# Performance work log

Hardware: AMD Instinct MI355X
Metric: run time of the kernel (lower is better)

## Reference

```python
import jax, jax.numpy as jnp
import numpy as np

WINDOW = 5  # len_sort_window in the original module


def setup_inputs() -> dict:
    key = jax.random.key(0)
    k1, k2, k3 = jax.random.split(key, 3)
    B, L, D = 8, 4000, 512  # L divisible by WINDOW, D < L
    q = jax.random.normal(k1, (B, L, D), dtype=jnp.float32)
    k = jax.random.normal(k2, (B, L, D), dtype=jnp.float32)
    v = jax.random.normal(k3, (B, L, D), dtype=jnp.float32)
    return {"q": q, "k": k, "v": v}


def reference(q, k, v):
    # q, k are unused by the original forward.
    B, L, D = v.shape
    t = jnp.arange(L)          # sequence positions
    s = jnp.arange(D)          # per-feature cyclic shift amount (= feature index)
    # Shift feature i left by i: shifted[:, t, i] = v[:, (t + i) % L, i]
    idx_fwd = (t[:, None] + s[None, :]) % L            # [L, D]
    v_shift = jnp.take_along_axis(v, idx_fwd[None, :, :], axis=1)  # [B, L, D]
    # Sort within fixed non-overlapping windows of size WINDOW along the seq axis.
    v_sorted = jnp.sort(v_shift.reshape(B, L // WINDOW, WINDOW, D), axis=2)
    v_sorted = v_sorted.reshape(B, L, D)
    # Unshift feature i right by i: out[:, t, i] = v_sorted[:, (t - i) % L, i]
    idx_bwd = (t[:, None] - s[None, :]) % L            # [L, D]
    return jnp.take_along_axis(v_sorted, idx_bwd[None, :, :], axis=1)
```

## Files before the change

### kernel.cpp

```cpp
#include <hip/hip_runtime.h>


constexpr int L  = 4000;
constexpr int D  = 512;
constexpr int SROWS   = 20;
constexpr int NSTRIPS = L / SROWS;

#define CE(a, b) { float lo_ = fminf(a, b); float hi_ = fmaxf(a, b); (a) = lo_; (b) = hi_; }

__global__ __launch_bounds__(256, 6)
void swd18_strip_scalar(const float* __restrict__ v, float* __restrict__ out) {
    const int nwg = gridDim.x * gridDim.y;
    const int lid = blockIdx.x + gridDim.x * blockIdx.y;
    const int q   = nwg >> 3;
    const int rm  = nwg & 7;
    const int xcd = lid & 7;
    const int pos = lid >> 3;
    const int nid = (xcd < rm ? xcd * (q + 1) : rm * (q + 1) + (xcd - rm) * q) + pos;

    const int b     = nid / (NSTRIPS * 2);
    const int rr    = nid % (NSTRIPS * 2);
    const int half  = rr & 1;
    const int strip = rr >> 1;
    const int i     = half * 256 + threadIdx.x;

    const float* __restrict__ vb = v   + (size_t)b * (L * D);
    float*       __restrict__ ob = out + (size_t)b * (L * D);

    const int R0 = strip * SROWS;

    float r[30];
    {
        int row = R0 - 5; if (row < 0) row += L;
#pragma unroll
        for (int j = 0; j < 5; ++j)
            r[j] = vb[(size_t)(row + j) * D + i];
    }
#pragma unroll
    for (int j = 5; j < 25; ++j)
        r[j] = vb[(size_t)(R0 + j - 5) * D + i];
    {
        int row = R0 + 20; if (row >= L) row -= L;
#pragma unroll
        for (int j = 25; j < 30; ++j)
            r[j] = vb[(size_t)(row + j - 25) * D + i];
    }

    const int rc = i % 5;
    const bool e0 = rc == 0, e1 = rc == 1, e2 = rc == 2, e3 = rc == 3;

#pragma unroll
    for (int k = 0; k < 4; ++k) {
        const float* p = &r[5 * k];

        float A0 = e0 ? p[0] : e1 ? p[1] : e2 ? p[2] : e3 ? p[3] : p[4];
        float A1 = e0 ? p[1] : e1 ? p[2] : e2 ? p[3] : e3 ? p[4] : p[5];
        float A2 = e0 ? p[2] : e1 ? p[3] : e2 ? p[4] : e3 ? p[5] : p[6];
        float A3 = e0 ? p[3] : e1 ? p[4] : e2 ? p[5] : e3 ? p[6] : p[7];
        float A4 = e0 ? p[4] : e1 ? p[5] : e2 ? p[6] : e3 ? p[7] : p[8];
        float B0 = e0 ? p[5] : e1 ? p[6] : e2 ? p[7] : e3 ? p[8] : p[9];
        float B1 = e0 ? p[6] : e1 ? p[7] : e2 ? p[8] : e3 ? p[9] : p[10];
        float B2 = e0 ? p[7] : e1 ? p[8] : e2 ? p[9] : e3 ? p[10] : p[11];
        float B3 = e0 ? p[8] : e1 ? p[9] : e2 ? p[10] : e3 ? p[11] : p[12];
        float B4 = e0 ? p[9] : e1 ? p[10] : e2 ? p[11] : e3 ? p[12] : p[13];

        CE(A0, A1) CE(A3, A4) CE(A2, A4) CE(A2, A3) CE(A1, A4)
        CE(A0, A3) CE(A0, A2) CE(A1, A3) CE(A1, A2)
        CE(B0, B1) CE(B3, B4) CE(B2, B4) CE(B2, B3) CE(B1, B4)
        CE(B0, B3) CE(B0, B2) CE(B1, B3) CE(B1, B2)

        float f0 = e0 ? B0 : e1 ? A4 : e2 ? A3 : e3 ? A2 : A1;
        float f1 = e0 ? B1 : e1 ? B0 : e2 ? A4 : e3 ? A3 : A2;
        float f2 = e0 ? B2 : e1 ? B1 : e2 ? B0 : e3 ? A4 : A3;
        float f3 = e0 ? B3 : e1 ? B2 : e2 ? B1 : e3 ? B0 : A4;
        float f4 = e0 ? B4 : e1 ? B3 : e2 ? B2 : e3 ? B1 : B0;

        float* o = ob + (size_t)(R0 + 5 * k) * D + i;
        __builtin_nontemporal_store(f0, o + 0 * D);
        __builtin_nontemporal_store(f1, o + 1 * D);
        __builtin_nontemporal_store(f2, o + 2 * D);
        __builtin_nontemporal_store(f3, o + 3 * D);
        __builtin_nontemporal_store(f4, o + 4 * D);
    }
}

#undef CE

extern "C" void kernel_launch(void* const* d_in, const int* in_sizes, int n_in,
                              void* d_out, int out_size, void* d_ws, size_t ws_size,
                              hipStream_t stream) {
    const float* v = (const float*)d_in[2];
    float* out = (float*)d_out;

    const int B = in_sizes[2] / (L * D);
    dim3 grid(NSTRIPS * 2, B);
    swd18_strip_scalar<<<grid, dim3(256), 0, stream>>>(v, out);
}
```

Measured before the change: 179.9 us.

## Process taller strips with a rolling register ring of row groups

Each workgroup now handles 50 rows instead of 20. Five-row groups stream through a 5-slot register ring, and the next group is prefetched while the current one is sorted. This cuts the redundant halo reads from 50% extra per strip to 20% and gives each thread more work, at the cost of fewer workgroups (fewer waves to spread across CUs) and possibly more registers live at once.

New measurement: 181.4 us. About the same (+0.8%).

```diff
diff --git a/kernel.cpp b/kernel.cpp
--- a/kernel.cpp
+++ b/kernel.cpp
@@ -3,13 +3,14 @@
 
 constexpr int L  = 4000;
 constexpr int D  = 512;
-constexpr int SROWS   = 20;
+constexpr int SROWS   = 50;
+constexpr int NG      = SROWS / 5;
 constexpr int NSTRIPS = L / SROWS;
 
 #define CE(a, b) { float lo_ = fminf(a, b); float hi_ = fmaxf(a, b); (a) = lo_; (b) = hi_; }
 
 __global__ __launch_bounds__(256, 6)
-void swd18_strip_scalar(const float* __restrict__ v, float* __restrict__ out) {
+void swd18_ring(const float* __restrict__ v, float* __restrict__ out) {
     const int nwg = gridDim.x * gridDim.y;
     const int lid = blockIdx.x + gridDim.x * blockIdx.y;
     const int q   = nwg >> 3;
@@ -29,40 +30,44 @@
 
     const int R0 = strip * SROWS;
 
-    float r[30];
-    {
-        int row = R0 - 5; if (row < 0) row += L;
+    float s[5][5];
+
+    auto loadg = [&](int slot, int g) {
+        int row = R0 + 5 * g;
+        if (row < 0)  row += L;
+        if (row >= L) row -= L;
 #pragma unroll
         for (int j = 0; j < 5; ++j)
-            r[j] = vb[(size_t)(row + j) * D + i];
-    }
-#pragma unroll
-    for (int j = 5; j < 25; ++j)
-        r[j] = vb[(size_t)(R0 + j - 5) * D + i];
-    {
-        int row = R0 + 20; if (row >= L) row -= L;
-#pragma unroll
-        for (int j = 25; j < 30; ++j)
-            r[j] = vb[(size_t)(row + j - 25) * D + i];
-    }
+            s[slot][j] = vb[(size_t)(row + j) * D + i];
+    };
+
+    loadg(0, -1);
+    loadg(1,  0);
+    loadg(2,  1);
+    loadg(3,  2);
 
     const int rc = i % 5;
     const bool e0 = rc == 0, e1 = rc == 1, e2 = rc == 2, e3 = rc == 3;
 
 #pragma unroll
-    for (int k = 0; k < 4; ++k) {
-        const float* p = &r[5 * k];
+    for (int k = 0; k < NG; ++k) {
+        if (k + 3 <= NG)
+            loadg((k + 4) % 5, k + 3);
 
-        float A0 = e0 ? p[0] : e1 ? p[1] : e2 ? p[2] : e3 ? p[3] : p[4];
-        float A1 = e0 ? p[1] : e1 ? p[2] : e2 ? p[3] : e3 ? p[4] : p[5];
-        float A2 = e0 ? p[2] : e1 ? p[3] : e2 ? p[4] : e3 ? p[5] : p[6];
-        float A3 = e0 ? p[3] : e1 ? p[4] : e2 ? p[5] : e3 ? p[6] : p[7];
-        float A4 = e0 ? p[4] : e1 ? p[5] : e2 ? p[6] : e3 ? p[7] : p[8];
-        float B0 = e0 ? p[5] : e1 ? p[6] : e2 ? p[7] : e3 ? p[8] : p[9];
-        float B1 = e0 ? p[6] : e1 ? p[7] : e2 ? p[8] : e3 ? p[9] : p[10];
-        float B2 = e0 ? p[7] : e1 ? p[8] : e2 ? p[9] : e3 ? p[10] : p[11];
-        float B3 = e0 ? p[8] : e1 ? p[9] : e2 ? p[10] : e3 ? p[11] : p[12];
-        float B4 = e0 ? p[9] : e1 ? p[10] : e2 ? p[11] : e3 ? p[12] : p[13];
+        const float* P = s[k % 5];
+        const float* C = s[(k + 1) % 5];
+        const float* N = s[(k + 2) % 5];
+
+        float A0 = e0 ? P[0] : e1 ? P[1] : e2 ? P[2] : e3 ? P[3] : P[4];
+        float A1 = e0 ? P[1] : e1 ? P[2] : e2 ? P[3] : e3 ? P[4] : C[0];
+        float A2 = e0 ? P[2] : e1 ? P[3] : e2 ? P[4] : e3 ? C[0] : C[1];
+        float A3 = e0 ? P[3] : e1 ? P[4] : e2 ? C[0] : e3 ? C[1] : C[2];
+        float A4 = e0 ? P[4] : e1 ? C[0] : e2 ? C[1] : e3 ? C[2] : C[3];
+        float B0 = e0 ? C[0] : e1 ? C[1] : e2 ? C[2] : e3 ? C[3] : C[4];
+        float B1 = e0 ? C[1] : e1 ? C[2] : e2 ? C[3] : e3 ? C[4] : N[0];
+        float B2 = e0 ? C[2] : e1 ? C[3] : e2 ? C[4] : e3 ? N[0] : N[1];
+        float B3 = e0 ? C[3] : e1 ? C[4] : e2 ? N[0] : e3 ? N[1] : N[2];
+        float B4 = e0 ? C[4] : e1 ? N[0] : e2 ? N[1] : e3 ? N[2] : N[3];
 
         CE(A0, A1) CE(A3, A4) CE(A2, A4) CE(A2, A3) CE(A1, A4)
         CE(A0, A3) CE(A0, A2) CE(A1, A3) CE(A1, A2)
@@ -94,5 +99,5 @@
 
     const int B = in_sizes[2] / (L * D);
     dim3 grid(NSTRIPS * 2, B);
-    swd18_strip_scalar<<<grid, dim3(256), 0, stream>>>(v, out);
+    swd18_ring<<<grid, dim3(256), 0, stream>>>(v, out);
 }
```
